# Optimization experiments

Measured on AMD Instinct MI355X. Metric: run time of the kernel, lower is better.

The kernel has to match this reference:

```python
import jax, jax.numpy as jnp
import numpy as np
from jax import lax

N, CIN, COUT, K = 16, 3, 16, 3
D = H = W = 64

def setup_inputs() -> dict:
    key = jax.random.key(0)
    k1, k2, k3 = jax.random.split(key, 3)
    x = jax.random.normal(k1, (N, CIN, D, H, W), dtype=jnp.float32)
    # torch Conv3d default init scale ~ 1/sqrt(fan_in); plain normals are fine for a baseline
    fan_in = CIN * K * K * K
    weight = jax.random.normal(k2, (COUT, CIN, K, K, K), dtype=jnp.float32) / np.sqrt(fan_in)
    bias = jax.random.normal(k3, (COUT,), dtype=jnp.float32) * 0.01
    return {"x": x, "weight": weight, "bias": bias}

def reference(x, weight, bias):
    # Conv3d, stride 1, no padding (NCDHW / OIDHW)
    y = lax.conv_general_dilated(
        x, weight,
        window_strides=(1, 1, 1),
        padding="VALID",
        dimension_numbers=("NCDHW", "OIDHW", "NCDHW"),
    )
    y = y + bias[None, :, None, None, None]          # [N, C, D', H', W']
    m = jnp.min(y, axis=2)                            # min over D -> [N, C, H', W']
    return jax.nn.softmax(m, axis=1)                  # softmax over channels
```

## Files before the change

kernel.cpp:

```cpp
#include <hip/hip_runtime.h>
#include <math.h>


#define CH 4

__global__ __launch_bounds__(1024)
void conv3d_min_softmax(
    const float* __restrict__ x,
    const float* __restrict__ wgt,
    const float* __restrict__ bias,
    float* __restrict__ out)
{
    const int tid = threadIdx.x;
    const int wv  = __builtin_amdgcn_readfirstlane(tid >> 6);
    const int l   = tid & 63;
    const int r0  = l >> 3;
    const int cg  = l & 7;
    const int wc  = cg * 4;
    const int n   = blockIdx.z;
    const int h0  = blockIdx.y * 8;
    const int w0  = blockIdx.x * 32;

    __shared__ __align__(16) float sx[2][4320];
    __shared__ float sm[256 * 17];

    const float bv = bias[wv];

    int goff[2];
#pragma unroll
    for (int k = 0; k < 2; ++k) {
        int F = tid + 1024 * k;
        if (F > 1079) F = 1079;
        int ci  = F / 360;
        int rem = F - ci * 360;
        int dd  = rem / 90;
        int rr  = rem - dd * 90;
        int rw  = rr / 9;
        int g   = rr - rw * 9;
        int gh  = h0 + rw;  if (gh > 63) gh = 63;
        int gw  = w0 + g * 4; if (gw > 60) gw = 60;
        goff[k] = (((ci * 64 + dd) * 64 + gh) * 64 + gw) * 4;
    }
    const char* xb = (const char*)(x + (size_t)n * 3 * 64 * 64 * 64);

    float Aacc[6][4];
#pragma unroll
    for (int j = 0; j < 6; ++j)
#pragma unroll
        for (int p = 0; p < 4; ++p) Aacc[j][p] = 0.f;
    float mv[4] = {1e30f, 1e30f, 1e30f, 1e30f};

    {
        char* lb = (char*)&sx[0][0];
        __builtin_amdgcn_global_load_lds(
            (const void*)(xb + goff[0]), (void*)(lb + tid * 16), 16, 0, 0);
        if (tid < 56)
            __builtin_amdgcn_global_load_lds(
                (const void*)(xb + goff[1]),
                (void*)(lb + (1024 + tid) * 16), 16, 0, 0);
    }

    for (int c = 0; c < 64 / CH; ++c) {
        __syncthreads();

        if (c < 64 / CH - 1) {
            const char* xc = xb + (size_t)(c + 1) * (CH * 64 * 64 * 4);
            char* lb = (char*)&sx[(c + 1) & 1][0];
            __builtin_amdgcn_global_load_lds(
                (const void*)(xc + goff[0]), (void*)(lb + tid * 16),
                16, 0, 0);
            if (tid < 56)
                __builtin_amdgcn_global_load_lds(
                    (const void*)(xc + goff[1]),
                    (void*)(lb + (1024 + tid) * 16), 16, 0, 0);
        }

        const float* S = sx[c & 1];

#pragma unroll 1
        for (int ci = 0; ci < 3; ++ci) {
            float wsc[27];
            {
                const float* wp_ = wgt + (wv * 3 + ci) * 27;
#pragma unroll
                for (int i = 0; i < 27; ++i) wsc[i] = wp_[i];
            }
            const float* Sci = S + ci * (CH * 10 * 36) + r0 * 36 + wc;
#pragma unroll
            for (int dd = 0; dd < CH; ++dd) {
#pragma unroll
                for (int kh = 0; kh < 3; ++kh) {
                    const float4 a = *(const float4*)&Sci[(dd * 10 + kh) * 36];
                    const float2 b =
                        *(const float2*)&Sci[(dd * 10 + kh) * 36 + 4];
                    const float row[6] = {a.x, a.y, a.z, a.w, b.x, b.y};
#pragma unroll
                    for (int kw = 0; kw < 3; ++kw) {
                        const float wk0 = wsc[0  + kh * 3 + kw];
                        const float wk1 = wsc[9  + kh * 3 + kw];
                        const float wk2 = wsc[18 + kh * 3 + kw];
#pragma unroll
                        for (int p = 0; p < 4; ++p) {
                            const float xv = row[kw + p];
                            Aacc[dd + 2][p] = fmaf(xv, wk0, Aacc[dd + 2][p]);
                            Aacc[dd + 1][p] = fmaf(xv, wk1, Aacc[dd + 1][p]);
                            Aacc[dd + 0][p] = fmaf(xv, wk2, Aacc[dd + 0][p]);
                        }
                    }
                }
            }
        }

        const bool full = (c > 0);
#pragma unroll
        for (int j = 0; j < 4; ++j) {
            if (j >= 2 || full) {
#pragma unroll
                for (int p = 0; p < 4; ++p)
                    mv[p] = fminf(mv[p], Aacc[j][p]);
            }
        }
#pragma unroll
        for (int p = 0; p < 4; ++p) {
            Aacc[0][p] = Aacc[4][p];
            Aacc[1][p] = Aacc[5][p];
        }
#pragma unroll
        for (int j = 2; j < 6; ++j)
#pragma unroll
            for (int p = 0; p < 4; ++p) Aacc[j][p] = 0.f;
    }

    const int px0 = r0 * 32 + wc;
#pragma unroll
    for (int pp = 0; pp < 4; ++pp)
        sm[(px0 + pp) * 17 + wv] = mv[pp] + bv;
    __syncthreads();

    const int hp = h0 + r0;
#pragma unroll
    for (int pp = 0; pp < 4; ++pp) {
        const int px = px0 + pp;
        float mx = -1e30f;
#pragma unroll
        for (int j = 0; j < 16; ++j) mx = fmaxf(mx, sm[px * 17 + j]);
        float sum = 0.f;
#pragma unroll
        for (int j = 0; j < 16; ++j) sum += __expf(sm[px * 17 + j] - mx);
        const int wp = w0 + wc + pp;
        if (hp < 62 && wp < 62) {
            const float e = __expf(sm[px * 17 + wv] - mx);
            out[(((size_t)n * 16 + wv) * 62 + hp) * 62 + wp] = e / sum;
        }
    }
}

extern "C" void kernel_launch(void* const* d_in, const int* in_sizes, int n_in,
                              void* d_out, int out_size, void* d_ws, size_t ws_size,
                              hipStream_t stream) {
    const float* x    = (const float*)d_in[0];
    const float* wgt  = (const float*)d_in[1];
    const float* bias = (const float*)d_in[2];
    float* out        = (float*)d_out;
    dim3 grid(2, 8, 16);
    dim3 block(1024);
    hipLaunchKernelGGL(conv3d_min_softmax, grid, block, 0, stream,
                       x, wgt, bias, out);
}
```

Before: 245.9 us.

## Split depth reduction across two blocks with atomic min and separate softmax kernel

Each (n) slab is now split into two depth halves handled by separate blocks, doubling the grid so two blocks can share each CU. Partial minima are combined with atomicMin on an order-preserving unsigned encoding in the output buffer, which is first set to 0xFF by a memset. A second kernel decodes the values, adds the bias and runs the channel softmax with shuffles. The cost is a little redundant halo compute, a memset, an extra launch and atomics.

```diff
diff --git a/kernel.cpp b/kernel.cpp
--- a/kernel.cpp
+++ b/kernel.cpp
@@ -4,12 +4,20 @@
 
 #define CH 4
 
+__device__ __forceinline__ unsigned enc_min(float f) {
+    unsigned u = __float_as_uint(f);
+    return (u & 0x80000000u) ? ~u : (u | 0x80000000u);
+}
+__device__ __forceinline__ float dec_min(unsigned k) {
+    unsigned u = (k & 0x80000000u) ? (k ^ 0x80000000u) : ~k;
+    return __uint_as_float(u);
+}
+
 __global__ __launch_bounds__(1024)
-void conv3d_min_softmax(
+void conv3d_min_part(
     const float* __restrict__ x,
     const float* __restrict__ wgt,
-    const float* __restrict__ bias,
-    float* __restrict__ out)
+    unsigned* __restrict__ outk)
 {
     const int tid = threadIdx.x;
     const int wv  = __builtin_amdgcn_readfirstlane(tid >> 6);
@@ -17,14 +25,16 @@
     const int r0  = l >> 3;
     const int cg  = l & 7;
     const int wc  = cg * 4;
-    const int n   = blockIdx.z;
+    const int z   = blockIdx.z;
+    const int n   = z >> 1;
+    const int dh  = z & 1;
+    const int base = dh * 28;
+    const int lo  = dh * 30;
+    const int hi  = lo + 31;
     const int h0  = blockIdx.y * 8;
     const int w0  = blockIdx.x * 32;
 
     __shared__ __align__(16) float sx[2][4320];
-    __shared__ float sm[256 * 17];
-
-    const float bv = bias[wv];
 
     int goff[2];
 #pragma unroll
@@ -39,7 +49,7 @@
         int g   = rr - rw * 9;
         int gh  = h0 + rw;  if (gh > 63) gh = 63;
         int gw  = w0 + g * 4; if (gw > 60) gw = 60;
-        goff[k] = (((ci * 64 + dd) * 64 + gh) * 64 + gw) * 4;
+        goff[k] = (((ci * 64 + base + dd) * 64 + gh) * 64 + gw) * 4;
     }
     const char* xb = (const char*)(x + (size_t)n * 3 * 64 * 64 * 64);
 
@@ -60,10 +70,10 @@
                 (void*)(lb + (1024 + tid) * 16), 16, 0, 0);
     }
 
-    for (int c = 0; c < 64 / CH; ++c) {
+    for (int c = 0; c < 9; ++c) {
         __syncthreads();
 
-        if (c < 64 / CH - 1) {
+        if (c < 8) {
             const char* xc = xb + (size_t)(c + 1) * (CH * 64 * 64 * 4);
             char* lb = (char*)&sx[(c + 1) & 1][0];
             __builtin_amdgcn_global_load_lds(
@@ -111,10 +121,10 @@
             }
         }
 
-        const bool full = (c > 0);
+        const int dpb = base + c * 4 - 2;
 #pragma unroll
         for (int j = 0; j < 4; ++j) {
-            if (j >= 2 || full) {
+            if (dpb + j >= lo && dpb + j <= hi) {
 #pragma unroll
                 for (int p = 0; p < 4; ++p)
                     mv[p] = fminf(mv[p], Aacc[j][p]);
@@ -131,28 +141,43 @@
             for (int p = 0; p < 4; ++p) Aacc[j][p] = 0.f;
     }
 
-    const int px0 = r0 * 32 + wc;
-#pragma unroll
-    for (int pp = 0; pp < 4; ++pp)
-        sm[(px0 + pp) * 17 + wv] = mv[pp] + bv;
-    __syncthreads();
-
     const int hp = h0 + r0;
 #pragma unroll
     for (int pp = 0; pp < 4; ++pp) {
-        const int px = px0 + pp;
-        float mx = -1e30f;
+        const int wp = w0 + wc + pp;
+        if (hp < 62 && wp < 62)
+            atomicMin(&outk[(((size_t)n * 16 + wv) * 62 + hp) * 62 + wp],
+                      enc_min(mv[pp]));
+    }
+}
+
+__global__ __launch_bounds__(256)
+void softmax_fin(
+    unsigned* __restrict__ outk,
+    const float* __restrict__ bias)
+{
+    const int tid = threadIdx.x;
+    const int c   = tid & 15;
+    const int pxi = blockIdx.x * 16 + (tid >> 4);
+    const int n   = pxi / 3844;
+    const int rem = pxi - n * 3844;
+    const int hp  = rem / 62;
+    const int wp  = rem - hp * 62;
+
+    const size_t idx = (((size_t)n * 16 + c) * 62 + hp) * 62 + wp;
+    float v = dec_min(outk[idx]) + bias[c];
+
+    float mx = v;
 #pragma unroll
-        for (int j = 0; j < 16; ++j) mx = fmaxf(mx, sm[px * 17 + j]);
-        float sum = 0.f;
+    for (int off = 1; off < 16; off <<= 1)
+        mx = fmaxf(mx, __shfl_xor(mx, off, 64));
+    float e = __expf(v - mx);
+    float sum = e;
 #pragma unroll
-        for (int j = 0; j < 16; ++j) sum += __expf(sm[px * 17 + j] - mx);
-        const int wp = w0 + wc + pp;
-        if (hp < 62 && wp < 62) {
-            const float e = __expf(sm[px * 17 + wv] - mx);
-            out[(((size_t)n * 16 + wv) * 62 + hp) * 62 + wp] = e / sum;
-        }
-    }
+    for (int off = 1; off < 16; off <<= 1)
+        sum += __shfl_xor(sum, off, 64);
+
+    ((float*)outk)[idx] = e / sum;
 }
 
 extern "C" void kernel_launch(void* const* d_in, const int* in_sizes, int n_in,
@@ -161,9 +186,14 @@
     const float* x    = (const float*)d_in[0];
     const float* wgt  = (const float*)d_in[1];
     const float* bias = (const float*)d_in[2];
-    float* out        = (float*)d_out;
-    dim3 grid(2, 8, 16);
-    dim3 block(1024);
-    hipLaunchKernelGGL(conv3d_min_softmax, grid, block, 0, stream,
-                       x, wgt, bias, out);
+
+    hipMemsetAsync(d_out, 0xFF, (size_t)out_size * sizeof(float), stream);
+
+    dim3 g1(2, 8, 32);
+    hipLaunchKernelGGL(conv3d_min_part, g1, dim3(1024), 0, stream,
+                       x, wgt, (unsigned*)d_out);
+
+    dim3 g2(3844);
+    hipLaunchKernelGGL(softmax_fin, g2, dim3(256), 0, stream,
+                       (unsigned*)d_out, bias);
 }
```

Result: slower. 285.3 us (+16.0%).

## Remap per-thread work to two output channels by two pixels

Applied to the files above, without the earlier changes.

Each wave now covers two output channels and half of the 8-row tile, so a thread computes 2 pixels for 2 channels instead of 4 pixels for 1 channel. Each LDS input value is reused across two channels' weights rather than across more pixels, and each thread reads 4 floats per row instead of 6. This trades LDS traffic per FMA and uses twice as many scalar weight loads per thread. Register pressure is about the same, but the overlap between neighbouring pixel windows is smaller.

```diff
diff --git a/kernel.cpp b/kernel.cpp
--- a/kernel.cpp
+++ b/kernel.cpp
@@ -12,19 +12,20 @@
     float* __restrict__ out)
 {
     const int tid = threadIdx.x;
-    const int wv  = __builtin_amdgcn_readfirstlane(tid >> 6);
-    const int l   = tid & 63;
-    const int r0  = l >> 3;
-    const int cg  = l & 7;
-    const int wc  = cg * 4;
-    const int n   = blockIdx.z;
-    const int h0  = blockIdx.y * 8;
-    const int w0  = blockIdx.x * 32;
+    const int wv   = __builtin_amdgcn_readfirstlane(tid >> 6);
+    const int half = wv & 1;
+    const int co0  = (wv >> 1) * 2;
+    const int co1  = co0 + 1;
+    const int l    = tid & 63;
+    const int r0   = half * 4 + (l >> 4);
+    const int cg   = l & 15;
+    const int wc   = cg * 2;
+    const int n    = blockIdx.z;
+    const int h0   = blockIdx.y * 8;
+    const int w0   = blockIdx.x * 32;
 
     __shared__ __align__(16) float sx[2][4320];
     __shared__ float sm[256 * 17];
-
-    const float bv = bias[wv];
 
     int goff[2];
 #pragma unroll
@@ -43,12 +44,13 @@
     }
     const char* xb = (const char*)(x + (size_t)n * 3 * 64 * 64 * 64);
 
-    float Aacc[6][4];
+    float A0acc[6][2], A1acc[6][2];
 #pragma unroll
     for (int j = 0; j < 6; ++j)
 #pragma unroll
-        for (int p = 0; p < 4; ++p) Aacc[j][p] = 0.f;
-    float mv[4] = {1e30f, 1e30f, 1e30f, 1e30f};
+        for (int p = 0; p < 2; ++p) { A0acc[j][p] = 0.f; A1acc[j][p] = 0.f; }
+    float mv0[2] = {1e30f, 1e30f};
+    float mv1[2] = {1e30f, 1e30f};
 
     {
         char* lb = (char*)&sx[0][0];
@@ -60,10 +62,10 @@
                 (void*)(lb + (1024 + tid) * 16), 16, 0, 0);
     }
 
-    for (int c = 0; c < 64 / CH; ++c) {
+    for (int c = 0; c < 16; ++c) {
         __syncthreads();
 
-        if (c < 64 / CH - 1) {
+        if (c < 15) {
             const char* xc = xb + (size_t)(c + 1) * (CH * 64 * 64 * 4);
             char* lb = (char*)&sx[(c + 1) & 1][0];
             __builtin_amdgcn_global_load_lds(
@@ -79,32 +81,39 @@
 
 #pragma unroll 1
         for (int ci = 0; ci < 3; ++ci) {
-            float wsc[27];
+            float ws0[27], ws1[27];
             {
-                const float* wp_ = wgt + (wv * 3 + ci) * 27;
+                const float* wp0 = wgt + (co0 * 3 + ci) * 27;
+                const float* wp1 = wgt + (co1 * 3 + ci) * 27;
 #pragma unroll
-                for (int i = 0; i < 27; ++i) wsc[i] = wp_[i];
+                for (int i = 0; i < 27; ++i) { ws0[i] = wp0[i]; ws1[i] = wp1[i]; }
             }
             const float* Sci = S + ci * (CH * 10 * 36) + r0 * 36 + wc;
 #pragma unroll
             for (int dd = 0; dd < CH; ++dd) {
 #pragma unroll
                 for (int kh = 0; kh < 3; ++kh) {
-                    const float4 a = *(const float4*)&Sci[(dd * 10 + kh) * 36];
+                    const float2 a = *(const float2*)&Sci[(dd * 10 + kh) * 36];
                     const float2 b =
-                        *(const float2*)&Sci[(dd * 10 + kh) * 36 + 4];
-                    const float row[6] = {a.x, a.y, a.z, a.w, b.x, b.y};
+                        *(const float2*)&Sci[(dd * 10 + kh) * 36 + 2];
+                    const float row[4] = {a.x, a.y, b.x, b.y};
 #pragma unroll
                     for (int kw = 0; kw < 3; ++kw) {
-                        const float wk0 = wsc[0  + kh * 3 + kw];
-                        const float wk1 = wsc[9  + kh * 3 + kw];
-                        const float wk2 = wsc[18 + kh * 3 + kw];
+                        const float w00 = ws0[0  + kh * 3 + kw];
+                        const float w01 = ws0[9  + kh * 3 + kw];
+                        const float w02 = ws0[18 + kh * 3 + kw];
+                        const float w10 = ws1[0  + kh * 3 + kw];
+                        const float w11 = ws1[9  + kh * 3 + kw];
+                        const float w12 = ws1[18 + kh * 3 + kw];
 #pragma unroll
-                        for (int p = 0; p < 4; ++p) {
+                        for (int p = 0; p < 2; ++p) {
                             const float xv = row[kw + p];
-                            Aacc[dd + 2][p] = fmaf(xv, wk0, Aacc[dd + 2][p]);
-                            Aacc[dd + 1][p] = fmaf(xv, wk1, Aacc[dd + 1][p]);
-                            Aacc[dd + 0][p] = fmaf(xv, wk2, Aacc[dd + 0][p]);
+                            A0acc[dd + 2][p] = fmaf(xv, w00, A0acc[dd + 2][p]);
+                            A0acc[dd + 1][p] = fmaf(xv, w01, A0acc[dd + 1][p]);
+                            A0acc[dd + 0][p] = fmaf(xv, w02, A0acc[dd + 0][p]);
+                            A1acc[dd + 2][p] = fmaf(xv, w10, A1acc[dd + 2][p]);
+                            A1acc[dd + 1][p] = fmaf(xv, w11, A1acc[dd + 1][p]);
+                            A1acc[dd + 0][p] = fmaf(xv, w12, A1acc[dd + 0][p]);
                         }
                     }
                 }
@@ -116,30 +125,36 @@
         for (int j = 0; j < 4; ++j) {
             if (j >= 2 || full) {
 #pragma unroll
-                for (int p = 0; p < 4; ++p)
-                    mv[p] = fminf(mv[p], Aacc[j][p]);
+                for (int p = 0; p < 2; ++p) {
+                    mv0[p] = fminf(mv0[p], A0acc[j][p]);
+                    mv1[p] = fminf(mv1[p], A1acc[j][p]);
+                }
             }
         }
 #pragma unroll
-        for (int p = 0; p < 4; ++p) {
-            Aacc[0][p] = Aacc[4][p];
-            Aacc[1][p] = Aacc[5][p];
+        for (int p = 0; p < 2; ++p) {
+            A0acc[0][p] = A0acc[4][p]; A0acc[1][p] = A0acc[5][p];
+            A1acc[0][p] = A1acc[4][p]; A1acc[1][p] = A1acc[5][p];
         }
 #pragma unroll
         for (int j = 2; j < 6; ++j)
 #pragma unroll
-            for (int p = 0; p < 4; ++p) Aacc[j][p] = 0.f;
+            for (int p = 0; p < 2; ++p) { A0acc[j][p] = 0.f; A1acc[j][p] = 0.f; }
     }
 
+    const float bv0 = bias[co0];
+    const float bv1 = bias[co1];
     const int px0 = r0 * 32 + wc;
 #pragma unroll
-    for (int pp = 0; pp < 4; ++pp)
-        sm[(px0 + pp) * 17 + wv] = mv[pp] + bv;
+    for (int pp = 0; pp < 2; ++pp) {
+        sm[(px0 + pp) * 17 + co0] = mv0[pp] + bv0;
+        sm[(px0 + pp) * 17 + co1] = mv1[pp] + bv1;
+    }
     __syncthreads();
 
     const int hp = h0 + r0;
 #pragma unroll
-    for (int pp = 0; pp < 4; ++pp) {
+    for (int pp = 0; pp < 2; ++pp) {
         const int px = px0 + pp;
         float mx = -1e30f;
 #pragma unroll
@@ -149,8 +164,10 @@
         for (int j = 0; j < 16; ++j) sum += __expf(sm[px * 17 + j] - mx);
         const int wp = w0 + wc + pp;
         if (hp < 62 && wp < 62) {
-            const float e = __expf(sm[px * 17 + wv] - mx);
-            out[(((size_t)n * 16 + wv) * 62 + hp) * 62 + wp] = e / sum;
+            const float e0 = __expf(sm[px * 17 + co0] - mx);
+            const float e1 = __expf(sm[px * 17 + co1] - mx);
+            out[(((size_t)n * 16 + co0) * 62 + hp) * 62 + wp] = e0 / sum;
+            out[(((size_t)n * 16 + co1) * 62 + hp) * 62 + wp] = e1 / sum;
         }
     }
 }
```

New measurement: 198.8 us. 19.1% less time.
